# Kernel optimization log

Hardware: AMD Instinct MI355X
Metric: run time of the kernel (lower is better)

## Reference

```python
import jax, jax.numpy as jnp
import numpy as np

N_PRED = 10000
N_GT = 1000
NUM_CLASSES = 80
IMG_H = 800
IMG_W = 1333
EPS = 1e-12
ALPHA, GAMMA, CLS_W = 0.25, 2.0, 2.0
L1_W, IOU_W = 5.0, 2.0
CENTER_RADIUS = 2.5
CAND_TOPK = 5


def _make_boxes(key, n, w, h):
    k1, k2 = jax.random.split(key)
    cxcy = jax.random.uniform(k1, (n, 2)) * jnp.array([w, h], jnp.float32)
    wh = jax.random.uniform(k2, (n, 2)) * 190.0 + 10.0
    return jnp.concatenate([cxcy - wh / 2, cxcy + wh / 2], axis=1).astype(jnp.float32)


def setup_inputs() -> dict:
    key = jax.random.key(0)
    k1, k2, k3, k4 = jax.random.split(key, 4)
    return {
        'pred_logits': jax.random.normal(k1, (N_PRED, NUM_CLASSES), jnp.float32),
        'pred_boxes': _make_boxes(k2, N_PRED, IMG_W, IMG_H),
        'gt_bboxes': _make_boxes(k3, N_GT, IMG_W, IMG_H),
        'gt_labels': jax.random.randint(k4, (N_GT,), 0, NUM_CLASSES),
        'img_h': IMG_H,
        'img_w': IMG_W,
    }


def _pairwise_iou_giou(pred, gt):
    area_p = (pred[:, 2] - pred[:, 0]) * (pred[:, 3] - pred[:, 1])
    area_g = (gt[:, 2] - gt[:, 0]) * (gt[:, 3] - gt[:, 1])
    lt = jnp.maximum(pred[:, None, :2], gt[None, :, :2])
    rb = jnp.minimum(pred[:, None, 2:], gt[None, :, 2:])
    wh = jnp.clip(rb - lt, 0.0)
    inter = wh[..., 0] * wh[..., 1]                       # [N,G]
    union = area_p[:, None] + area_g[None, :] - inter
    iou = inter / jnp.maximum(union, EPS)
    elt = jnp.minimum(pred[:, None, :2], gt[None, :, :2])
    erb = jnp.maximum(pred[:, None, 2:], gt[None, :, 2:])
    ewh = jnp.clip(erb - elt, 0.0)
    enclose = ewh[..., 0] * ewh[..., 1]
    giou = iou - (enclose - union) / jnp.maximum(enclose, EPS)
    return iou, giou


def _center_info(pred, gt):
    # pred/gt in xyxy; uses pred box centers, strict inequalities as in source
    pcx = (pred[:, 0] + pred[:, 2]) * 0.5
    pcy = (pred[:, 1] + pred[:, 3]) * 0.5
    gx1, gy1, gx2, gy2 = gt[:, 0], gt[:, 1], gt[:, 2], gt[:, 3]
    in_boxes = ((pcx[:, None] > gx1) & (pcx[:, None] < gx2) &
                (pcy[:, None] > gy1) & (pcy[:, None] < gy2))
    gcx, gcy = (gx1 + gx2) * 0.5, (gy1 + gy2) * 0.5
    gw, gh = gx2 - gx1, gy2 - gy1
    r = CENTER_RADIUS
    in_centers = ((pcx[:, None] > gcx - r * gw) & (pcx[:, None] < gcx + r * gw) &
                  (pcy[:, None] > gcy - r * gh) & (pcy[:, None] < gcy + r * gh))
    valid = in_boxes.any(1) | in_centers.any(1)
    return valid, in_boxes & in_centers


def _compute_cost_and_ious(pred_logits, pred_boxes, gt_bboxes, gt_labels, img_h, img_w):
    # FocalLossCost
    p = jax.nn.sigmoid(pred_logits)
    neg = -jnp.log1p(-(p - EPS)) * (1 - ALPHA) * p ** GAMMA
    pos = -jnp.log(p + EPS) * ALPHA * (1 - p) ** GAMMA
    cls_cost = (pos - neg)[:, gt_labels] * CLS_W            # [N,G]
    # BBoxL1Cost (normalized by image size)
    factor = jnp.array([img_w, img_h, img_w, img_h], jnp.float32)
    l1_cost = jnp.sum(jnp.abs(pred_boxes[:, None, :] / factor -
                              gt_bboxes[None, :, :] / factor), -1) * L1_W
    # IoUCost (giou) + pairwise ious for dynamic-k
    ious, giou = _pairwise_iou_giou(pred_boxes, gt_bboxes)
    iou_cost = -giou * IOU_W
    valid_mask, in_boxes_and_center = _center_info(pred_boxes, gt_bboxes)
    cost = cls_cost + l1_cost + iou_cost + jnp.where(in_boxes_and_center, 0.0, 100.0)
    cost = cost + jnp.where(valid_mask, 0.0, 10000.0)[:, None]
    return cost, ious


def _dynamic_k_matching(cost, ious):
    n, g = cost.shape
    k = min(CAND_TOPK, n)
    topk_ious, _ = jax.lax.top_k(ious.T, k)                 # [G,k]
    dynamic_ks = jnp.maximum(topk_ious.sum(1).astype(jnp.int32), 1)
    _, idx = jax.lax.top_k(-cost.T, k)                      # [G,k] smallest costs per gt
    vals = (jnp.arange(k)[None, :] < dynamic_ks[:, None]).astype(cost.dtype)
    cols = jnp.broadcast_to(jnp.arange(g)[:, None], (g, k))
    mm = jnp.zeros_like(cost).at[idx, cols].max(vals)       # scatter 1s per gt column
    # resolve priors matched to >1 gt (note: mask is reused stale inside the loop, as in source)
    prior_mask = mm.sum(1) > 1
    cmin = jnp.argmin(cost, axis=1)
    mm = jnp.where(prior_mask[:, None], jax.nn.one_hot(cmin, g, dtype=cost.dtype), mm)

    def cond(state):
        m, _ = state
        return jnp.any(m.sum(0) == 0)

    def body(state):
        m, c = state
        matched_q = m.sum(1) > 0
        c = c + 100000.0 * matched_q[:, None].astype(c.dtype)
        unmatched = m.sum(0) == 0
        pos = jnp.argmin(c, axis=0)                         # [G]
        oh = jax.nn.one_hot(pos, n, dtype=c.dtype).T        # [N,G]
        m = jnp.where(unmatched[None, :], oh, m)
        cmin2 = jnp.argmin(c, axis=1)
        m_fix = jnp.where(prior_mask[:, None], jax.nn.one_hot(cmin2, g, dtype=c.dtype), m)
        m = jnp.where(jnp.any(m.sum(1) > 1), m_fix, m)
        return (m, c)

    mm, _ = jax.lax.while_loop(cond, body, (mm, cost))
    fg_mask = mm.sum(1) > 0
    matched = jnp.argmax(mm, axis=1).astype(jnp.int32)
    return fg_mask, jnp.where(fg_mask, matched, 0)


def reference(pred_logits, pred_boxes, gt_bboxes, gt_labels, img_h, img_w):
    cost, ious = _compute_cost_and_ious(pred_logits, pred_boxes, gt_bboxes,
                                        gt_labels, img_h, img_w)
    fg_mask, matched_gt = _dynamic_k_matching(cost, ious)
    # dense form: matched_gt[i] valid only where fg_mask[i] (fixed-shape version of
    # the original's compressed matched_gt_inds = mm[fg_mask].argmax(1))
    return fg_mask, matched_gt
```

## Files before the change

kernel.cpp:

```cpp
#include <hip/hip_runtime.h>
#include <cfloat>
#include <cmath>

#define NP 10000
#define NG 1000
#define NC 80
#define LMAX 6
#define NCH 2
#define CHSZ (NP / NCH)
#define MAIN_IT 19
#define TAIL_N  136

#define S_MULTI 12
#define S_BODY  16
#define RI_BIG  0x3fffffff
#define KMAX    0xFFFFFFFFFFFFFFFFull

__device__ __forceinline__ bool lexless(float av, int ai, float bv, int bi) {
    return (av < bv) || (av == bv && ai < bi);
}

__device__ __forceinline__ unsigned long long packkey(float v, int idx) {
    unsigned u = __float_as_uint(v);
    u ^= (unsigned)(((int)u) >> 31) | 0x80000000u;
    return ((unsigned long long)u << 32) | (unsigned)idx;
}
__device__ __forceinline__ int keyidx(unsigned long long k) {
    return (int)(unsigned)(k & 0xFFFFFFFFu);
}

__device__ __forceinline__ float inflate(float c, int k) {
    for (int q = 0; q < k; q++) c += 100000.0f;
    return c;
}

__device__ __forceinline__ void cost_iou(float4 p, float4 pn, float4 pi,
        float4 g, float4 cb, float4 Gn, float ga, float clsv,
        float& cc_out, float& iou_out) {
#pragma clang fp contract(off)
    float wx = fminf(p.z, g.z) - fmaxf(p.x, g.x); wx = fmaxf(wx, 0.0f);
    float wy = fminf(p.w, g.w) - fmaxf(p.y, g.y); wy = fmaxf(wy, 0.0f);
    float inter = wx * wy;
    float uni = pi.z + ga - inter;
    float iou = inter / fmaxf(uni, 1e-12f);
    float ex = fmaxf(p.z, g.z) - fminf(p.x, g.x); ex = fmaxf(ex, 0.0f);
    float ey = fmaxf(p.w, g.w) - fminf(p.y, g.y); ey = fmaxf(ey, 0.0f);
    float enc = ex * ey;
    float giou = iou - (enc - uni) / fmaxf(enc, 1e-12f);
    float l1 = ((fabsf(pn.x - Gn.x) + fabsf(pn.y - Gn.y))
                + fabsf(pn.z - Gn.z)) + fabsf(pn.w - Gn.w);
    float cc = clsv + l1 * 5.0f;
    cc = cc + (-giou * 2.0f);
    bool inb = (pi.x > g.x && pi.x < g.z && pi.y > g.y && pi.y < g.w);
    bool inc = (pi.x > cb.x && pi.x < cb.z && pi.y > cb.y && pi.y < cb.w);
    cc = cc + ((inb && inc) ? 0.0f : 100.0f);
    cc = cc + pi.w;
    cc_out = cc; iou_out = iou;
}

#define CLS_TI 64
#define PB_CLS0 40
#define PB_G0   197
#define PB_V0   201
__global__ __launch_bounds__(256) void k_prep(const float* __restrict__ logits,
        const float* __restrict__ pb, const float* __restrict__ gb,
        const int* __restrict__ imgw, const int* __restrict__ imgh,
        float* __restrict__ clsval, float4* __restrict__ pnorm,
        float4* __restrict__ pinfo, float4* __restrict__ gcb,
        float4* __restrict__ gnm, float* __restrict__ gar,
        int* rowcnt, int* rowfirst, int* rowiter, int* prior, int* priorcol,
        int* colsum, int* scal)
{
    __shared__ float sl[CLS_TI * (NC + 1)];
    int b = blockIdx.x;
    if (b < PB_CLS0) {
        int i = b * 256 + threadIdx.x;
        if (i < NP) {
            rowcnt[i] = 0; rowfirst[i] = 0x7fffffff; rowiter[i] = RI_BIG;
            prior[i] = 0; priorcol[i] = 0;
        }
        if (i < NG) colsum[i] = 0;
        if (i < 32) scal[i] = 0;
    } else if (b < PB_G0) {
        int i0 = (b - PB_CLS0) * CLS_TI;
        bool full = (i0 + CLS_TI) <= NP;
        if (full) {
            const float* src = logits + (size_t)i0 * NC;
            for (int e = threadIdx.x; e < CLS_TI * NC; e += 256) {
                int di = e / NC, c = e - di * NC;
                sl[di * (NC + 1) + c] = src[e];
            }
        } else {
            for (int e = threadIdx.x; e < CLS_TI * NC; e += 256) {
                int di = e / NC, c = e - di * NC;
                int i = i0 + di;
                sl[di * (NC + 1) + c] = (i < NP) ? logits[(size_t)i * NC + c] : 0.0f;
            }
        }
        __syncthreads();
        for (int e = threadIdx.x; e < CLS_TI * NC; e += 256) {
            int c = e >> 6, di = e & 63;
            int i = i0 + di;
            if (i >= NP) continue;
            float x = sl[di * (NC + 1) + c];
            float p = 1.0f / (1.0f + expf(-x));
            float neg = -log1pf(-(p - 1e-12f)) * 0.75f * (p * p);
            float om = 1.0f - p;
            float pos = -logf(p + 1e-12f) * 0.25f * (om * om);
            clsval[(size_t)c * NP + i] = (pos - neg) * 2.0f;
        }
    } else if (b < PB_V0) {
#pragma clang fp contract(off)
        int j = (b - PB_G0) * 256 + threadIdx.x;
        if (j < NG) {
            float fw = (float)imgw[0], fh = (float)imgh[0];
            float4 g = ((const float4*)gb)[j];
            float gcx = (g.x + g.z) * 0.5f, gcy = (g.y + g.w) * 0.5f;
            float gw = g.z - g.x, gh = g.w - g.y;
            float4 cb; cb.x = gcx - 2.5f * gw; cb.y = gcy - 2.5f * gh;
            cb.z = gcx + 2.5f * gw; cb.w = gcy + 2.5f * gh;
            gcb[j] = cb;
            float4 Gn; Gn.x = g.x / fw; Gn.y = g.y / fh; Gn.z = g.z / fw; Gn.w = g.w / fh;
            gnm[j] = Gn;
            gar[j] = (g.z - g.x) * (g.w - g.y);
        }
    } else {
#pragma clang fp contract(off)
        int wave = threadIdx.x >> 6;
        int lane = threadIdx.x & 63;
        int i = (b - PB_V0) * 4 + wave;
        if (i >= NP) return;
        float4 p = ((const float4*)pb)[i];
        float pcx = (p.x + p.z) * 0.5f, pcy = (p.y + p.w) * 0.5f;
        int vb = 0, vc = 0;
        const float4* gb4 = (const float4*)gb;
        for (int j = lane; j < NG; j += 64) {
            float4 g = gb4[j];
            vb |= (pcx > g.x && pcx < g.z && pcy > g.y && pcy < g.w) ? 1 : 0;
            float gcx = (g.x + g.z) * 0.5f, gcy = (g.y + g.w) * 0.5f;
            float gw = g.z - g.x, gh = g.w - g.y;
            vc |= (pcx > gcx - 2.5f * gw && pcx < gcx + 2.5f * gw &&
                   pcy > gcy - 2.5f * gh && pcy < gcy + 2.5f * gh) ? 1 : 0;
        }
        int any = (__any(vb) ? 1 : 0) | (__any(vc) ? 1 : 0);
        if (lane == 0) {
            float fw = (float)imgw[0], fh = (float)imgh[0];
            float4 pn; pn.x = p.x / fw; pn.y = p.y / fh; pn.z = p.z / fw; pn.w = p.w / fh;
            pnorm[i] = pn;
            float4 pi4; pi4.x = pcx; pi4.y = pcy;
            pi4.z = (p.z - p.x) * (p.w - p.y);
            pi4.w = any ? 0.0f : 10000.0f;
            pinfo[i] = pi4;
        }
    }
}

__global__ __launch_bounds__(256) void k_cost2(
        const float* __restrict__ pb, const float* __restrict__ gb,
        const int* __restrict__ glab, const float* __restrict__ clsval,
        const float4* __restrict__ pnorm, const float4* __restrict__ pinfo,
        const float4* __restrict__ gcb, const float4* __restrict__ gnm,
        const float* __restrict__ gar,
        unsigned long long* __restrict__ pck, float* __restrict__ piv)
{
    __shared__ unsigned long long s_k[256 * 7];
    __shared__ float s_iv[256 * 7];
    __shared__ int s_bad;

    int j = blockIdx.x >> 1;
    int c = blockIdx.x & 1;
    int tid = threadIdx.x;
    if (tid == 0) s_bad = 0;
    float4 g  = ((const float4*)gb)[j];
    float4 cb = gcb[j];
    float4 Gn = gnm[j];
    float  ga = gar[j];
    const float* clscol = clsval + (size_t)glab[j] * NP;
    const float4* pb4 = (const float4*)pb;
    int base_i = c * CHSZ;

    unsigned long long k0 = KMAX, k1 = KMAX;
    float i0 = -1.0f, i1 = -1.0f;
#pragma unroll 4
    for (int k = 0; k < MAIN_IT; k++) {
        int i = base_i + tid + k * 256;
        float cc, iou;
        cost_iou(pb4[i], pnorm[i], pinfo[i], g, cb, Gn, ga, clscol[i], cc, iou);
        unsigned long long key = packkey(cc, i);
        unsigned long long mx = (k0 > key) ? k0 : key;
        k0 = (k0 > key) ? key : k0;
        k1 = (k1 > mx) ? mx : k1;
        float mnv = fminf(i0, iou);
        i0 = fmaxf(i0, iou);
        i1 = fmaxf(i1, mnv);
    }
    if (tid < TAIL_N) {
        int i = base_i + MAIN_IT * 256 + tid;
        float cc, iou;
        cost_iou(pb4[i], pnorm[i], pinfo[i], g, cb, Gn, ga, clscol[i], cc, iou);
        unsigned long long key = packkey(cc, i);
        unsigned long long mx = (k0 > key) ? k0 : key;
        k0 = (k0 > key) ? key : k0;
        k1 = (k1 > mx) ? mx : k1;
        float mnv = fminf(i0, iou);
        i0 = fmaxf(i0, iou);
        i1 = fmaxf(i1, mnv);
    }

    int base = tid * 7;
    s_k[base+0] = k0; s_k[base+1] = k1;
    s_k[base+2] = KMAX; s_k[base+3] = KMAX; s_k[base+4] = KMAX; s_k[base+5] = KMAX;
    s_iv[base+0] = i0; s_iv[base+1] = i1;
    s_iv[base+2] = -2.0f; s_iv[base+3] = -2.0f; s_iv[base+4] = -2.0f; s_iv[base+5] = -2.0f;
    __syncthreads();

    for (int w = 128; w > 0; w >>= 1) {
        if (tid < w) {
            int a = tid * 7, bb = (tid + w) * 7;
            unsigned long long ok[5]; float og[5];
            int pa = a, pbp = bb;
#pragma unroll
            for (int t = 0; t < 5; t++) {
                unsigned long long A = s_k[pa], B = s_k[pbp];
                if (A <= B) { ok[t] = A; pa++; } else { ok[t] = B; pbp++; }
            }
            int qa = a, qb = bb;
#pragma unroll
            for (int t = 0; t < 5; t++) {
                float A = s_iv[qa], B = s_iv[qb];
                if (A >= B) { og[t] = A; qa++; } else { og[t] = B; qb++; }
            }
#pragma unroll
            for (int t = 0; t < 5; t++) { s_k[a+t] = ok[t]; s_iv[a+t] = og[t]; }
        }
        __syncthreads();
    }

    if (k1 < s_k[4] || i1 > s_iv[4]) s_bad = 1;
    __syncthreads();

    if (s_bad) {
        unsigned long long kv[5]; float iv[5];
#pragma unroll
        for (int t = 0; t < 5; t++) { kv[t] = KMAX; iv[t] = -1.0f; }
        for (int k = 0; k <= MAIN_IT; k++) {
            if (k == MAIN_IT && tid >= TAIL_N) break;
            int i = base_i + tid + k * 256;
            float cc, iou;
            cost_iou(pb4[i], pnorm[i], pinfo[i], g, cb, Gn, ga, clscol[i], cc, iou);
            unsigned long long key = packkey(cc, i);
            if (key < kv[4]) {
                kv[4] = key;
#pragma unroll
                for (int t = 4; t > 0; t--)
                    if (kv[t] < kv[t-1]) { unsigned long long tv = kv[t]; kv[t] = kv[t-1]; kv[t-1] = tv; }
            }
            if (iou > iv[4]) {
                iv[4] = iou;
#pragma unroll
                for (int t = 4; t > 0; t--)
                    if (iv[t] > iv[t-1]) { float tv = iv[t]; iv[t] = iv[t-1]; iv[t-1] = tv; }
            }
        }
#pragma unroll
        for (int t = 0; t < 5; t++) { s_k[base+t] = kv[t]; s_iv[base+t] = iv[t]; }
        s_k[base+5] = KMAX; s_iv[base+5] = -2.0f;
        __syncthreads();
        for (int w = 128; w > 0; w >>= 1) {
            if (tid < w) {
                int a = tid * 7, bb = (tid + w) * 7;
                unsigned long long ok[5]; float og[5];
                int pa = a, pbp = bb;
#pragma unroll
                for (int t = 0; t < 5; t++) {
                    unsigned long long A = s_k[pa], B = s_k[pbp];
                    if (A <= B) { ok[t] = A; pa++; } else { ok[t] = B; pbp++; }
                }
                int qa = a, qb = bb;
#pragma unroll
                for (int t = 0; t < 5; t++) {
                    float A = s_iv[qa], B = s_iv[qb];
                    if (A >= B) { og[t] = A; qa++; } else { og[t] = B; qb++; }
                }
#pragma unroll
                for (int t = 0; t < 5; t++) { s_k[a+t] = ok[t]; s_iv[a+t] = og[t]; }
            }
            __syncthreads();
        }
    }

    if (tid == 0) {
        int ob = blockIdx.x * 5;
#pragma unroll
        for (int t = 0; t < 5; t++) { pck[ob + t] = s_k[t]; piv[ob + t] = s_iv[t]; }
    }
}

__global__ __launch_bounds__(256) void k_costmerge(
        const unsigned long long* __restrict__ pck, const float* __restrict__ piv,
        int* __restrict__ rowcnt, int* __restrict__ rowfirst,
        int* __restrict__ rowiter, int* __restrict__ top5,
        int* __restrict__ dkarr)
{
    int j = blockIdx.x * 256 + threadIdx.x;
    if (j >= NG) return;
    int base = j * 2 * 5;
    int h0 = 0, h1 = 0;
    int besti[5];
#pragma unroll
    for (int r = 0; r < 5; r++) {
        unsigned long long v0 = pck[base + h0];
        unsigned long long v1 = pck[base + 5 + h1];
        if (v0 <= v1) { besti[r] = keyidx(v0); h0++; }
        else          { besti[r] = keyidx(v1); h1++; }
    }
    int g0 = 0, g1 = 0;
    float ivm[5];
#pragma unroll
    for (int r = 0; r < 5; r++) {
        float v0 = piv[base + g0];
        float v1 = piv[base + 5 + g1];
        if (v0 >= v1) { ivm[r] = v0; g0++; } else { ivm[r] = v1; g1++; }
    }
    float s = (((ivm[0] + ivm[1]) + ivm[2]) + ivm[3]) + ivm[4];
    int dk = (int)s;
    if (dk < 1) dk = 1;
    dkarr[j] = dk;
#pragma unroll
    for (int r = 0; r < 5; r++) top5[j * 5 + r] = besti[r];
    for (int t = 0; t < dk; t++) {
        int r = besti[t];
        atomicAdd(&rowcnt[r], 1);
        atomicMin(&rowfirst[r], j);
        atomicMin(&rowiter[r], -1);
    }
}

__global__ __launch_bounds__(256) void k_pfixsurv(const float* __restrict__ pb,
        const float* __restrict__ gb, const int* __restrict__ glab,
        const float* __restrict__ clsval,
        const float4* __restrict__ pnorm, const float4* __restrict__ pinfo,
        const float4* __restrict__ gcb, const float4* __restrict__ gnm,
        const float* __restrict__ gar,
        int* __restrict__ prior, int* __restrict__ priorcol,
        int* __restrict__ colsum,
        const int* __restrict__ rowcnt, const int* __restrict__ top5,
        const int* __restrict__ dkarr)
{
    int b = blockIdx.x;
    int tid = threadIdx.x;
    if (b >= 2500) {
        int j = (b - 2500) * 256 + tid;
        if (j >= NG) return;
        int c = 0;
        int dk = dkarr[j];
        for (int t = 0; t < dk; t++) if (rowcnt[top5[j * 5 + t]] == 1) c++;
        if (c) atomicAdd(&colsum[j], c);
        return;
    }
    __shared__ float rv[256]; __shared__ int ri[256];
    for (int q = 0; q < 4; q++) {
        int row = b * 4 + q;
        if (rowcnt[row] <= 1) continue;
        if (tid == 0) prior[row] = 1;
        float4 p = ((const float4*)pb)[row];
        float4 pn = pnorm[row];
        float4 pi4 = pinfo[row];
        float best = FLT_MAX; int bj = 0x7fffffff;
        for (int j = tid; j < NG; j += 256) {
            float cc, iou;
            cost_iou(p, pn, pi4, ((const float4*)gb)[j], gcb[j], gnm[j], gar[j],
                     clsval[(size_t)glab[j] * NP + row], cc, iou);
            if (lexless(cc, j, best, bj)) { best = cc; bj = j; }
        }
        rv[tid] = best; ri[tid] = bj; __syncthreads();
        for (int w = 128; w > 0; w >>= 1) {
            if (tid < w) {
                float ov = rv[tid + w]; int oi = ri[tid + w];
                if (lexless(ov, oi, rv[tid], ri[tid])) { rv[tid] = ov; ri[tid] = oi; }
            }
            __syncthreads();
        }
        if (tid == 0) {
            priorcol[row] = ri[0];
            atomicAdd(&colsum[ri[0]], 1);
        }
        __syncthreads();
    }
}

__global__ __launch_bounds__(256) void k_iterB(const float* __restrict__ pb,
        const float* __restrict__ gb, const int* __restrict__ glab,
        const float* __restrict__ clsval,
        const float4* __restrict__ pnorm, const float4* __restrict__ pinfo,
        const float4* __restrict__ gcb, const float4* __restrict__ gnm,
        const float* __restrict__ gar, const int* __restrict__ top5,
        int* __restrict__ rowiter, int* __restrict__ rowcnt,
        int* __restrict__ rowfirst, int* __restrict__ colsum,
        int* __restrict__ scal, int t)
{
    int j = blockIdx.x;
    if (colsum[j] != 0) return;
    int tid = threadIdx.x;
    if (tid == 0) scal[S_BODY + t] = 1;

    __shared__ int s_pos;
    if (tid == 0) {
        int pos = -1;
        for (int r = 0; r < 5; r++) {
            int i = top5[j * 5 + r];
            if (rowiter[i] >= t) { pos = i; break; }
        }
        s_pos = pos;
    }
    __syncthreads();
    int pos = s_pos;

    if (pos < 0) {
        float4 g  = ((const float4*)gb)[j];
        float4 cb = gcb[j];
        float4 Gn = gnm[j];
        float  ga = gar[j];
        const float* clscol = clsval + (size_t)glab[j] * NP;
        const float4* pb4 = (const float4*)pb;
        __shared__ float rv[256]; __shared__ int ri[256];
        float best = FLT_MAX; int bi = 0x7fffffff;
        for (int i = tid; i < NP; i += 256) {
            if (rowiter[i] < t) continue;
            float cc, iou;
            cost_iou(pb4[i], pnorm[i], pinfo[i], g, cb, Gn, ga, clscol[i], cc, iou);
            if (lexless(cc, i, best, bi)) { best = cc; bi = i; }
        }
        rv[tid] = best; ri[tid] = bi; __syncthreads();
        for (int w = 128; w > 0; w >>= 1) {
            if (tid < w) {
                float ov = rv[tid + w]; int oi = ri[tid + w];
                if (lexless(ov, oi, rv[tid], ri[tid])) { rv[tid] = ov; ri[tid] = oi; }
            }
            __syncthreads();
        }
        pos = ri[0];
    }

    if (tid == 0) {
        colsum[j] = 1;
        int old = atomicAdd(&rowcnt[pos], 1);
        if (old >= 1) scal[S_MULTI] = 1;
        atomicMin(&rowfirst[pos], j);
        atomicMin(&rowiter[pos], t);
    }
}

__global__ __launch_bounds__(256) void k_iterC(const float* __restrict__ pb,
        const float* __restrict__ gb, const int* __restrict__ glab,
        const float* __restrict__ clsval,
        const float4* __restrict__ pnorm, const float4* __restrict__ pinfo,
        const float4* __restrict__ gcb, const float4* __restrict__ gnm,
        const float* __restrict__ gar,
        const int* __restrict__ prior, const int* __restrict__ rowiter,
        int* __restrict__ priorcol, int* __restrict__ colsum,
        int* __restrict__ scal, int t)
{
    if (scal[S_BODY + t] == 0 || scal[S_MULTI] == 0) return;
    int b = blockIdx.x;
    int tid = threadIdx.x;
    __shared__ float rv[256]; __shared__ int ri[256];
    for (int q = 0; q < 4; q++) {
        int row = b * 4 + q;
        if (!prior[row]) continue;
        int k = t - rowiter[row]; if (k < 0) k = 0;
        float4 p = ((const float4*)pb)[row];
        float4 pn = pnorm[row];
        float4 pi4 = pinfo[row];
        float best = FLT_MAX; int bj = 0x7fffffff;
        for (int j = tid; j < NG; j += 256) {
            float cc, iou;
            cost_iou(p, pn, pi4, ((const float4*)gb)[j], gcb[j], gnm[j], gar[j],
                     clsval[(size_t)glab[j] * NP + row], cc, iou);
            float val = inflate(cc, k);
            if (lexless(val, j, best, bj)) { best = val; bj = j; }
        }
        rv[tid] = best; ri[tid] = bj; __syncthreads();
        for (int w = 128; w > 0; w >>= 1) {
            if (tid < w) {
                float ov = rv[tid + w]; int oi = ri[tid + w];
                if (lexless(ov, oi, rv[tid], ri[tid])) { rv[tid] = ov; ri[tid] = oi; }
            }
            __syncthreads();
        }
        if (tid == 0) {
            int nb = ri[0];
            int oldc = priorcol[row];
            if (nb != oldc) {
                atomicSub(&colsum[oldc], 1);
                atomicAdd(&colsum[nb], 1);
                priorcol[row] = nb;
            }
        }
        __syncthreads();
    }
}

__global__ __launch_bounds__(256) void k_final(const int* __restrict__ rowcnt,
        const int* __restrict__ prior, const int* __restrict__ priorcol,
        const int* __restrict__ rowfirst, int* __restrict__ out)
{
    int i = blockIdx.x * 256 + threadIdx.x;
    if (i >= NP) return;
    int fg = rowcnt[i] > 0;
    out[i] = fg ? 1 : 0;
    out[NP + i] = fg ? (prior[i] ? priorcol[i] : rowfirst[i]) : 0;
}

extern "C" void kernel_launch(void* const* d_in, const int* in_sizes, int n_in,
                              void* d_out, int out_size, void* d_ws, size_t ws_size,
                              hipStream_t stream)
{
    (void)in_sizes; (void)n_in; (void)out_size; (void)ws_size;
    const float* logits = (const float*)d_in[0];
    const float* pboxes = (const float*)d_in[1];
    const float* gboxes = (const float*)d_in[2];
    const int*   glab   = (const int*)d_in[3];
    const int*   imgh   = (const int*)d_in[4];
    const int*   imgw   = (const int*)d_in[5];
    int* out = (int*)d_out;

    char* w = (char*)d_ws;
    float*  clsval  = (float*)(w);
    float4* pnorm   = (float4*)(w + 3200000);
    float4* pinfo   = (float4*)(w + 3360000);
    float4* gcb     = (float4*)(w + 3520000);
    float4* gnm     = (float4*)(w + 3536000);
    float*  gar     = (float*)(w + 3552000);
    int* rowcnt     = (int*)(w + 3556000);
    int* rowfirst   = (int*)(w + 3596000);
    int* rowiter    = (int*)(w + 3636000);
    int* prior      = (int*)(w + 3676000);
    int* priorcol   = (int*)(w + 3716000);
    int* top5       = (int*)(w + 3756000);
    int* dkarr      = (int*)(w + 3776000);
    int* colsum     = (int*)(w + 3780000);
    int* scal       = (int*)(w + 3784000);
    unsigned long long* pck = (unsigned long long*)(w + 3784128);
    float* piv      = (float*)(w + 3864128);

    hipLaunchKernelGGL(k_prep, dim3(2701), dim3(256), 0, stream,
                       logits, pboxes, gboxes, imgw, imgh,
                       clsval, pnorm, pinfo, gcb, gnm, gar,
                       rowcnt, rowfirst, rowiter, prior, priorcol, colsum, scal);
    hipLaunchKernelGGL(k_cost2, dim3(NG * NCH), dim3(256), 0, stream,
                       pboxes, gboxes, glab, clsval, pnorm, pinfo, gcb, gnm, gar,
                       pck, piv);
    hipLaunchKernelGGL(k_costmerge, dim3(4), dim3(256), 0, stream,
                       pck, piv, rowcnt, rowfirst, rowiter, top5, dkarr);
    hipLaunchKernelGGL(k_pfixsurv, dim3(2504), dim3(256), 0, stream,
                       pboxes, gboxes, glab, clsval, pnorm, pinfo, gcb, gnm, gar,
                       prior, priorcol, colsum, rowcnt, top5, dkarr);
    for (int t = 0; t < LMAX; t++) {
        hipLaunchKernelGGL(k_iterB, dim3(NG), dim3(256), 0, stream,
                           pboxes, gboxes, glab, clsval, pnorm, pinfo, gcb, gnm, gar,
                           top5, rowiter, rowcnt, rowfirst, colsum, scal, t);
        hipLaunchKernelGGL(k_iterC, dim3(2500), dim3(256), 0, stream,
                           pboxes, gboxes, glab, clsval, pnorm, pinfo, gcb, gnm, gar,
                           prior, rowiter, priorcol, colsum, scal, t);
    }
    hipLaunchKernelGGL(k_final, dim3(40), dim3(256), 0, stream,
                       rowcnt, prior, priorcol, rowfirst, out);
}
```

Before: 166.4 us.

## Fuse cost merge into cost kernel and cache per-row top-8 for iterC

Removes the separate k_costmerge launch: the second block of each gt column to finish, chosen with an atomic ticket, performs the top-5 merge and dynamic-k row updates inside k_cost2. In k_pfixsurv each conflicted row now keeps a top-8 list of (cost, gt) pairs instead of only the argmin, and k_iterC reuses that list to find the inflated-cost argmin without recomputing 1000 costs, falling back to the full scan only when the 8th entry cannot rule out other columns. This is meant to cut one kernel launch and most of the repeated per-row cost recomputation across the six iterations. In exchange it adds a wider shared-memory merge in k_pfixsurv, extra global writes, and threadfence/atomic traffic in k_cost2.

```diff
diff --git a/kernel.cpp b/kernel.cpp
--- a/kernel.cpp
+++ b/kernel.cpp
@@ -27,6 +27,11 @@
 }
 __device__ __forceinline__ int keyidx(unsigned long long k) {
     return (int)(unsigned)(k & 0xFFFFFFFFu);
+}
+__device__ __forceinline__ float keyval(unsigned long long k) {
+    unsigned u = (unsigned)(k >> 32);
+    u = (u & 0x80000000u) ? (u ^ 0x80000000u) : ~u;
+    return __uint_as_float(u);
 }
 
 __device__ __forceinline__ float inflate(float c, int k) {
@@ -69,7 +74,7 @@
         float4* __restrict__ pinfo, float4* __restrict__ gcb,
         float4* __restrict__ gnm, float* __restrict__ gar,
         int* rowcnt, int* rowfirst, int* rowiter, int* prior, int* priorcol,
-        int* colsum, int* scal)
+        int* colsum, int* scal, int* done)
 {
     __shared__ float sl[CLS_TI * (NC + 1)];
     int b = blockIdx.x;
@@ -79,7 +84,7 @@
             rowcnt[i] = 0; rowfirst[i] = 0x7fffffff; rowiter[i] = RI_BIG;
             prior[i] = 0; priorcol[i] = 0;
         }
-        if (i < NG) colsum[i] = 0;
+        if (i < NG) { colsum[i] = 0; done[i] = 0; }
         if (i < 32) scal[i] = 0;
     } else if (b < PB_G0) {
         int i0 = (b - PB_CLS0) * CLS_TI;
@@ -161,7 +166,11 @@
         const float4* __restrict__ pnorm, const float4* __restrict__ pinfo,
         const float4* __restrict__ gcb, const float4* __restrict__ gnm,
         const float* __restrict__ gar,
-        unsigned long long* __restrict__ pck, float* __restrict__ piv)
+        unsigned long long* __restrict__ pck, float* __restrict__ piv,
+        int* __restrict__ done,
+        int* __restrict__ rowcnt, int* __restrict__ rowfirst,
+        int* __restrict__ rowiter, int* __restrict__ top5,
+        int* __restrict__ dkarr)
 {
     __shared__ unsigned long long s_k[256 * 7];
     __shared__ float s_iv[256 * 7];
@@ -293,46 +302,41 @@
         int ob = blockIdx.x * 5;
 #pragma unroll
         for (int t = 0; t < 5; t++) { pck[ob + t] = s_k[t]; piv[ob + t] = s_iv[t]; }
-    }
-}
-
-__global__ __launch_bounds__(256) void k_costmerge(
-        const unsigned long long* __restrict__ pck, const float* __restrict__ piv,
-        int* __restrict__ rowcnt, int* __restrict__ rowfirst,
-        int* __restrict__ rowiter, int* __restrict__ top5,
-        int* __restrict__ dkarr)
-{
-    int j = blockIdx.x * 256 + threadIdx.x;
-    if (j >= NG) return;
-    int base = j * 2 * 5;
-    int h0 = 0, h1 = 0;
-    int besti[5];
-#pragma unroll
-    for (int r = 0; r < 5; r++) {
-        unsigned long long v0 = pck[base + h0];
-        unsigned long long v1 = pck[base + 5 + h1];
-        if (v0 <= v1) { besti[r] = keyidx(v0); h0++; }
-        else          { besti[r] = keyidx(v1); h1++; }
-    }
-    int g0 = 0, g1 = 0;
-    float ivm[5];
-#pragma unroll
-    for (int r = 0; r < 5; r++) {
-        float v0 = piv[base + g0];
-        float v1 = piv[base + 5 + g1];
-        if (v0 >= v1) { ivm[r] = v0; g0++; } else { ivm[r] = v1; g1++; }
-    }
-    float s = (((ivm[0] + ivm[1]) + ivm[2]) + ivm[3]) + ivm[4];
-    int dk = (int)s;
-    if (dk < 1) dk = 1;
-    dkarr[j] = dk;
-#pragma unroll
-    for (int r = 0; r < 5; r++) top5[j * 5 + r] = besti[r];
-    for (int t = 0; t < dk; t++) {
-        int r = besti[t];
-        atomicAdd(&rowcnt[r], 1);
-        atomicMin(&rowfirst[r], j);
-        atomicMin(&rowiter[r], -1);
+        __threadfence();
+        int ticket = atomicAdd(&done[j], 1);
+        if (ticket == 1) {
+            __threadfence();
+            int mb = j * 2 * 5;
+            int h0 = 0, h1 = 0;
+            int besti[5];
+#pragma unroll
+            for (int r = 0; r < 5; r++) {
+                unsigned long long v0 = pck[mb + h0];
+                unsigned long long v1 = pck[mb + 5 + h1];
+                if (v0 <= v1) { besti[r] = keyidx(v0); h0++; }
+                else          { besti[r] = keyidx(v1); h1++; }
+            }
+            int g0 = 0, g1 = 0;
+            float ivm[5];
+#pragma unroll
+            for (int r = 0; r < 5; r++) {
+                float v0 = piv[mb + g0];
+                float v1 = piv[mb + 5 + g1];
+                if (v0 >= v1) { ivm[r] = v0; g0++; } else { ivm[r] = v1; g1++; }
+            }
+            float s = (((ivm[0] + ivm[1]) + ivm[2]) + ivm[3]) + ivm[4];
+            int dk = (int)s;
+            if (dk < 1) dk = 1;
+            dkarr[j] = dk;
+#pragma unroll
+            for (int r = 0; r < 5; r++) top5[j * 5 + r] = besti[r];
+            for (int t = 0; t < dk; t++) {
+                int r = besti[t];
+                atomicAdd(&rowcnt[r], 1);
+                atomicMin(&rowfirst[r], j);
+                atomicMin(&rowiter[r], -1);
+            }
+        }
     }
 }
 
@@ -345,7 +349,8 @@
         int* __restrict__ prior, int* __restrict__ priorcol,
         int* __restrict__ colsum,
         const int* __restrict__ rowcnt, const int* __restrict__ top5,
-        const int* __restrict__ dkarr)
+        const int* __restrict__ dkarr,
+        float* __restrict__ ptv, int* __restrict__ pti)
 {
     int b = blockIdx.x;
     int tid = threadIdx.x;
@@ -358,7 +363,7 @@
         if (c) atomicAdd(&colsum[j], c);
         return;
     }
-    __shared__ float rv[256]; __shared__ int ri[256];
+    __shared__ unsigned long long s_k[256 * 9];
     for (int q = 0; q < 4; q++) {
         int row = b * 4 + q;
         if (rowcnt[row] <= 1) continue;
@@ -366,24 +371,52 @@
         float4 p = ((const float4*)pb)[row];
         float4 pn = pnorm[row];
         float4 pi4 = pinfo[row];
-        float best = FLT_MAX; int bj = 0x7fffffff;
+
+        unsigned long long kv[4] = { KMAX, KMAX, KMAX, KMAX };
         for (int j = tid; j < NG; j += 256) {
             float cc, iou;
             cost_iou(p, pn, pi4, ((const float4*)gb)[j], gcb[j], gnm[j], gar[j],
                      clsval[(size_t)glab[j] * NP + row], cc, iou);
-            if (lexless(cc, j, best, bj)) { best = cc; bj = j; }
-        }
-        rv[tid] = best; ri[tid] = bj; __syncthreads();
+            unsigned long long key = packkey(cc, j);
+            if (key < kv[3]) {
+                kv[3] = key;
+#pragma unroll
+                for (int t = 3; t > 0; t--)
+                    if (kv[t] < kv[t-1]) { unsigned long long tv = kv[t]; kv[t] = kv[t-1]; kv[t-1] = tv; }
+            }
+        }
+        int base = tid * 9;
+#pragma unroll
+        for (int t = 0; t < 4; t++) s_k[base + t] = kv[t];
+#pragma unroll
+        for (int t = 4; t < 9; t++) s_k[base + t] = KMAX;
+        __syncthreads();
+
         for (int w = 128; w > 0; w >>= 1) {
             if (tid < w) {
-                float ov = rv[tid + w]; int oi = ri[tid + w];
-                if (lexless(ov, oi, rv[tid], ri[tid])) { rv[tid] = ov; ri[tid] = oi; }
+                int a = tid * 9, bb = (tid + w) * 9;
+                unsigned long long ok[8];
+                int pa = a, pbp = bb;
+#pragma unroll
+                for (int t = 0; t < 8; t++) {
+                    unsigned long long A = s_k[pa], B = s_k[pbp];
+                    if (A <= B) { ok[t] = A; pa++; } else { ok[t] = B; pbp++; }
+                }
+#pragma unroll
+                for (int t = 0; t < 8; t++) s_k[a + t] = ok[t];
             }
             __syncthreads();
         }
+
         if (tid == 0) {
-            priorcol[row] = ri[0];
-            atomicAdd(&colsum[ri[0]], 1);
+            int nb = keyidx(s_k[0]);
+            priorcol[row] = nb;
+            atomicAdd(&colsum[nb], 1);
+#pragma unroll
+            for (int r = 0; r < 8; r++) {
+                ptv[row * 8 + r] = keyval(s_k[r]);
+                pti[row * 8 + r] = keyidx(s_k[r]);
+            }
         }
         __syncthreads();
     }
@@ -458,6 +491,7 @@
         const float4* __restrict__ gcb, const float4* __restrict__ gnm,
         const float* __restrict__ gar,
         const int* __restrict__ prior, const int* __restrict__ rowiter,
+        const float* __restrict__ ptv, const int* __restrict__ pti,
         int* __restrict__ priorcol, int* __restrict__ colsum,
         int* __restrict__ scal, int t)
 {
@@ -469,27 +503,47 @@
         int row = b * 4 + q;
         if (!prior[row]) continue;
         int k = t - rowiter[row]; if (k < 0) k = 0;
-        float4 p = ((const float4*)pb)[row];
-        float4 pn = pnorm[row];
-        float4 pi4 = pinfo[row];
-        float best = FLT_MAX; int bj = 0x7fffffff;
-        for (int j = tid; j < NG; j += 256) {
-            float cc, iou;
-            cost_iou(p, pn, pi4, ((const float4*)gb)[j], gcb[j], gnm[j], gar[j],
-                     clsval[(size_t)glab[j] * NP + row], cc, iou);
-            float val = inflate(cc, k);
-            if (lexless(val, j, best, bj)) { best = val; bj = j; }
-        }
-        rv[tid] = best; ri[tid] = bj; __syncthreads();
-        for (int w = 128; w > 0; w >>= 1) {
-            if (tid < w) {
-                float ov = rv[tid + w]; int oi = ri[tid + w];
-                if (lexless(ov, oi, rv[tid], ri[tid])) { rv[tid] = ov; ri[tid] = oi; }
-            }
+
+        float wv = FLT_MAX; int wi = 0x7fffffff;
+        float i7 = 0.0f;
+#pragma unroll
+        for (int r = 0; r < 8; r++) {
+            float v = ptv[row * 8 + r];
+            int ix = pti[row * 8 + r];
+            float iv = inflate(v, k);
+            if (lexless(iv, ix, wv, wi)) { wv = iv; wi = ix; }
+            if (r == 7) i7 = iv;
+        }
+        bool safe = (i7 > wv);
+
+        int nb;
+        if (safe) {
+            nb = wi;
+        } else {
+            float4 p = ((const float4*)pb)[row];
+            float4 pn = pnorm[row];
+            float4 pi4 = pinfo[row];
+            float best = FLT_MAX; int bj = 0x7fffffff;
+            for (int j = tid; j < NG; j += 256) {
+                float cc, iou;
+                cost_iou(p, pn, pi4, ((const float4*)gb)[j], gcb[j], gnm[j], gar[j],
+                         clsval[(size_t)glab[j] * NP + row], cc, iou);
+                float val = inflate(cc, k);
+                if (lexless(val, j, best, bj)) { best = val; bj = j; }
+            }
+            rv[tid] = best; ri[tid] = bj; __syncthreads();
+            for (int w = 128; w > 0; w >>= 1) {
+                if (tid < w) {
+                    float ov = rv[tid + w]; int oi = ri[tid + w];
+                    if (lexless(ov, oi, rv[tid], ri[tid])) { rv[tid] = ov; ri[tid] = oi; }
+                }
+                __syncthreads();
+            }
+            nb = ri[0];
             __syncthreads();
         }
+
         if (tid == 0) {
-            int nb = ri[0];
             int oldc = priorcol[row];
             if (nb != oldc) {
                 atomicSub(&colsum[oldc], 1);
@@ -543,26 +597,27 @@
     int* scal       = (int*)(w + 3784000);
     unsigned long long* pck = (unsigned long long*)(w + 3784128);
     float* piv      = (float*)(w + 3864128);
+    int* done       = (int*)(w + 3904128);
+    float* ptv      = (float*)(w + 3908128);
+    int*   pti      = (int*)(w + 4228128);
 
     hipLaunchKernelGGL(k_prep, dim3(2701), dim3(256), 0, stream,
                        logits, pboxes, gboxes, imgw, imgh,
                        clsval, pnorm, pinfo, gcb, gnm, gar,
-                       rowcnt, rowfirst, rowiter, prior, priorcol, colsum, scal);
+                       rowcnt, rowfirst, rowiter, prior, priorcol, colsum, scal, done);
     hipLaunchKernelGGL(k_cost2, dim3(NG * NCH), dim3(256), 0, stream,
                        pboxes, gboxes, glab, clsval, pnorm, pinfo, gcb, gnm, gar,
-                       pck, piv);
-    hipLaunchKernelGGL(k_costmerge, dim3(4), dim3(256), 0, stream,
-                       pck, piv, rowcnt, rowfirst, rowiter, top5, dkarr);
+                       pck, piv, done, rowcnt, rowfirst, rowiter, top5, dkarr);
     hipLaunchKernelGGL(k_pfixsurv, dim3(2504), dim3(256), 0, stream,
                        pboxes, gboxes, glab, clsval, pnorm, pinfo, gcb, gnm, gar,
-                       prior, priorcol, colsum, rowcnt, top5, dkarr);
+                       prior, priorcol, colsum, rowcnt, top5, dkarr, ptv, pti);
     for (int t = 0; t < LMAX; t++) {
         hipLaunchKernelGGL(k_iterB, dim3(NG), dim3(256), 0, stream,
                            pboxes, gboxes, glab, clsval, pnorm, pinfo, gcb, gnm, gar,
                            top5, rowiter, rowcnt, rowfirst, colsum, scal, t);
         hipLaunchKernelGGL(k_iterC, dim3(2500), dim3(256), 0, stream,
                            pboxes, gboxes, glab, clsval, pnorm, pinfo, gcb, gnm, gar,
-                           prior, rowiter, priorcol, colsum, scal, t);
+                           prior, rowiter, ptv, pti, priorcol, colsum, scal, t);
     }
     hipLaunchKernelGGL(k_final, dim3(40), dim3(256), 0, stream,
                        rowcnt, prior, priorcol, rowfirst, out);
```

New measurement: 222.4 us. 33.6% more time.
